# Kernel tuning notes

Hardware: AMD Instinct MI355X
Metric: run time of the kernel (lower is better)

Reference implementation:

```python
import jax, jax.numpy as jnp
import numpy as np

B, S, D_FEAT, K_PER_ID = 128, 32, 256, 8   # PK sampling: 16 ids x 8 instances
MARGIN, K_AP, K_AN = 0.3, 3, 6
EPS = 1e-12


def setup_inputs() -> dict:
    key = jax.random.key(0)
    inputs = jax.random.normal(key, (B, S, D_FEAT), dtype=jnp.float32)
    # PK-structured labels: each identity appears exactly K_PER_ID times so every
    # anchor has the same number of positives/negatives (required by the reshape(b,-1)).
    targets = jnp.repeat(jnp.arange(B // K_PER_ID, dtype=jnp.int32), K_PER_ID)
    return {"inputs": inputs, "targets": targets}


def _phd_loss(inputs, targets):
    b, s, d = inputs.shape
    # F.normalize(p=2, dim=-1)
    x = inputs / jnp.maximum(jnp.linalg.norm(inputs, axis=-1, keepdims=True), EPS)
    X = x.reshape(b * s, d)
    # pairwise euclidean distances, (bs, bs)
    sq = jnp.sum(X * X, axis=1)
    dist = jnp.sqrt(jnp.clip(sq[:, None] + sq[None, :] - 2.0 * (X @ X.T), EPS, None))
    # as_strided block view: D[i*b+j] = dist[i*s:(i+1)*s, j*s:(j+1)*s]
    D = dist.reshape(b, s, b, s).transpose(0, 2, 1, 3).reshape(b * b, s, s)
    # positive / negative block indices (constants w.r.t. autodiff)
    tgt = np.asarray(targets)
    m = (tgt[:, None] == tgt[None, :]).reshape(-1)
    pos = np.nonzero(m)[0]    # b * K entries, grouped by anchor (row-major)
    neg = np.nonzero(~m)[0]   # b * (b - K) entries
    # set-to-set distances: min over frames of the other tracklet
    dij = jnp.min(D, axis=1)  # (b*b, s)
    dji = jnp.min(D, axis=2)  # (b*b, s)
    # hard positive: k_ap-th largest frame-min per positive block, max over ij/ji, max over positives
    ap_ij = jax.lax.top_k(dij[pos], K_AP)[0][:, -1]
    ap_ji = jax.lax.top_k(dji[pos], K_AP)[0][:, -1]
    dist_ap = jnp.max(jnp.maximum(ap_ij, ap_ji).reshape(b, -1), axis=1)
    # hard negative: k_an-th largest frame-min per negative block, min over ij/ji, min over negatives
    an_ij = jax.lax.top_k(dij[neg], K_AN)[0][:, -1]
    an_ji = jax.lax.top_k(dji[neg], K_AN)[0][:, -1]
    dist_an = jnp.min(jnp.minimum(an_ij, an_ji).reshape(b, -1), axis=1)
    # MarginRankingLoss(margin)(dist_an, dist_ap, y=1), reduction='mean'
    return jnp.mean(jax.nn.relu(dist_ap - dist_an + MARGIN))


def reference(inputs, targets):
    return _phd_loss(inputs, targets)
```

## Files before the change

### kernel.cpp

```cpp
#include <hip/hip_runtime.h>
#include <hip/hip_bf16.h>

#define NB 128
#define NS 32
#define DF 256
#define NROW (NB*NS)
#define KSTEPS (DF/16)
#define MARGIN 0.3f
#define PANEL (KSTEPS*64)
#define NPAIR (NB*(NB+1)/2)

typedef short bf16x8 __attribute__((ext_vector_type(8)));
typedef short bf16x4 __attribute__((ext_vector_type(4)));
typedef float f32x16 __attribute__((ext_vector_type(16)));

__device__ __forceinline__ short f2bf(float x) {
    unsigned u = __float_as_uint(x);
    u += 0x7fffu + ((u >> 16) & 1u);
    return (short)(u >> 16);
}

__global__ __launch_bounds__(64) void norm_kernel(const float* __restrict__ in,
                                                  short* __restrict__ Xhi) {
    const int row = blockIdx.x;
    const int lane = threadIdx.x;
    const float4 v = ((const float4*)(in + (size_t)row * DF))[lane];
    float s = v.x*v.x + v.y*v.y + v.z*v.z + v.w*v.w;
    #pragma unroll
    for (int off = 32; off; off >>= 1) s += __shfl_xor(s, off);
    const float inv = 1.0f / fmaxf(sqrtf(s), 1e-12f);
    const float o[4] = {v.x*inv, v.y*inv, v.z*inv, v.w*inv};

    const int trk = row >> 5, r32 = row & 31;
    const int k4 = lane * 4;
    const int ks = k4 >> 4;
    const int kq = k4 & 15;
    const int tl = ((kq >> 3) << 5) | r32;
    const size_t off8 = ((size_t)(trk * KSTEPS + ks) * 64 + tl) * 8 + (kq & 7);

    bf16x4 hv;
    #pragma unroll
    for (int c = 0; c < 4; c++) hv[c] = f2bf(o[c]);
    *(bf16x4*)(Xhi + off8) = hv;
}

__global__ __launch_bounds__(256) void pair_kernel(const short* __restrict__ Xhi,
                                                   const int* __restrict__ tgt,
                                                   float* __restrict__ val) {
    const int w = threadIdx.x >> 6;
    const int l = threadIdx.x & 63;
    const int h = l >> 5;
    const int idx = blockIdx.x * 4 + w;

    int i = (int)(128.5f - sqrtf(128.5f * 128.5f - 2.0f * (float)idx));
    while ((i + 1) * NB - ((i + 1) * i) / 2 <= idx) ++i;
    while (i * NB - (i * (i - 1)) / 2 > idx) --i;
    const int j = i + (idx - (i * NB - (i * (i - 1)) / 2));

    const bf16x8* P = (const bf16x8*)Xhi;
    const bf16x8* A = P + (size_t)i * PANEL + l;
    const bf16x8* B = P + (size_t)j * PANEL + l;

    f32x16 accF, accR;
    #pragma unroll
    for (int r = 0; r < 16; r++) { accF[r] = 0.0f; accR[r] = 0.0f; }

    #pragma unroll
    for (int ks = 0; ks < KSTEPS; ks++) {
        const bf16x8 a = A[ks * 64];
        const bf16x8 b = B[ks * 64];
        accF = __builtin_amdgcn_mfma_f32_32x32x16_bf16(a, b, accF, 0, 0, 0);
        accR = __builtin_amdgcn_mfma_f32_32x32x16_bf16(b, a, accR, 0, 0, 0);
    }

    const bool pos = (tgt[i] == tgt[j]);
    const int K = pos ? 3 : 6;

    float cf = accF[0], cr = accR[0];
    #pragma unroll
    for (int r = 1; r < 16; r++) { cf = fmaxf(cf, accF[r]); cr = fmaxf(cr, accR[r]); }
    cf = fmaxf(cf, __shfl_xor(cf, 32));
    cr = fmaxf(cr, __shfl_xor(cr, 32));

    __shared__ float buf[4][64];
    __shared__ float kv[4][2];
    buf[w][l] = h ? cr : cf;

    const float x = buf[w][l];
    const float* cb = &buf[w][h * 32];
    int c = 0, e = 0;
    #pragma unroll
    for (int q = 0; q < 8; q++) {
        const float4 y = *(const float4*)(cb + 4 * q);
        c += (y.x < x) + (y.y < x) + (y.z < x) + (y.w < x);
        e += (y.x == x) + (y.y == x) + (y.z == x) + (y.w == x);
    }
    if (c < K && c + e >= K) kv[w][h] = x;

    if (l == 0) {
        const float aij = kv[w][0], aji = kv[w][1];
        const float ac = pos ? fminf(aij, aji) : fmaxf(aij, aji);
        const float d = sqrtf(fmaxf(2.0f - 2.0f * ac, 1e-12f));
        val[i * NB + j] = d;
        val[j * NB + i] = d;
    }
}

__global__ __launch_bounds__(1024) void reduce_kernel(const float* __restrict__ val,
                                                      const int* __restrict__ tgt,
                                                      float* __restrict__ out) {
    __shared__ int   tg[NB];
    __shared__ float ls[NB];
    const int tid = threadIdx.x;
    if (tid < NB) tg[tid] = tgt[tid];
    __syncthreads();

    const int i = tid >> 3;
    const int g = tid & 7;
    const int ti = tg[i];
    float ap = -1e30f, an = 1e30f;
    const float4* vp = (const float4*)(val + i * NB + g * 16);
    #pragma unroll
    for (int q = 0; q < 4; q++) {
        const float4 v = vp[q];
        const int jb = g * 16 + q * 4;
        if (tg[jb + 0] == ti) ap = fmaxf(ap, v.x); else an = fminf(an, v.x);
        if (tg[jb + 1] == ti) ap = fmaxf(ap, v.y); else an = fminf(an, v.y);
        if (tg[jb + 2] == ti) ap = fmaxf(ap, v.z); else an = fminf(an, v.z);
        if (tg[jb + 3] == ti) ap = fmaxf(ap, v.w); else an = fminf(an, v.w);
    }
    #pragma unroll
    for (int off = 1; off < 8; off <<= 1) {
        ap = fmaxf(ap, __shfl_xor(ap, off));
        an = fminf(an, __shfl_xor(an, off));
    }
    if (g == 0) ls[i] = fmaxf(ap - an + MARGIN, 0.0f);
    __syncthreads();

    if (tid < 64) {
        float li = ls[tid] + ls[tid + 64];
        #pragma unroll
        for (int off = 32; off; off >>= 1) li += __shfl_xor(li, off);
        if (tid == 0) out[0] = li * (1.0f / (float)NB);
    }
}

extern "C" void kernel_launch(void* const* d_in, const int* in_sizes, int n_in,
                              void* d_out, int out_size, void* d_ws, size_t ws_size,
                              hipStream_t stream) {
    const float* in = (const float*)d_in[0];
    const int* tgt = (const int*)d_in[1];
    float* out = (float*)d_out;

    short* Xhi = (short*)d_ws;
    float* val = (float*)(Xhi + (size_t)NROW * DF);

    norm_kernel<<<NROW, 64, 0, stream>>>(in, Xhi);
    pair_kernel<<<NPAIR / 4, 256, 0, stream>>>(Xhi, tgt, val);
    reduce_kernel<<<1, 1024, 0, stream>>>(val, tgt, out);
}
```

Before: 26.18 us.

## Fuse reduction into pair kernel via last-block ticket and tile pairs in 2x2 superblocks

Removes the separate reduce kernel: each pair block increments an atomic counter and the last block to finish performs the final loss reduction. Pair work is regrouped so each block handles a 2x2 superblock of tracklet pairs, giving some L2/cache reuse of panels, and the norm kernel now packs four rows per block. A memset of the counter is added per launch. The superblock scheme computes some redundant diagonal pairs (i>j within diagonal superblocks), but these write symmetric values and so stay correct.

```diff
diff --git a/kernel.cpp b/kernel.cpp
--- a/kernel.cpp
+++ b/kernel.cpp
@@ -8,7 +8,8 @@
 #define KSTEPS (DF/16)
 #define MARGIN 0.3f
 #define PANEL (KSTEPS*64)
-#define NPAIR (NB*(NB+1)/2)
+#define NSUP (NB/2)
+#define NSBLK (NSUP*(NSUP+1)/2)
 
 typedef short bf16x8 __attribute__((ext_vector_type(8)));
 typedef short bf16x4 __attribute__((ext_vector_type(4)));
@@ -20,10 +21,10 @@
     return (short)(u >> 16);
 }
 
-__global__ __launch_bounds__(64) void norm_kernel(const float* __restrict__ in,
-                                                  short* __restrict__ Xhi) {
-    const int row = blockIdx.x;
-    const int lane = threadIdx.x;
+__global__ __launch_bounds__(256) void norm_kernel(const float* __restrict__ in,
+                                                   short* __restrict__ Xhi) {
+    const int row = blockIdx.x * 4 + (threadIdx.x >> 6);
+    const int lane = threadIdx.x & 63;
     const float4 v = ((const float4*)(in + (size_t)row * DF))[lane];
     float s = v.x*v.x + v.y*v.y + v.z*v.z + v.w*v.w;
     #pragma unroll
@@ -46,16 +47,20 @@
 
 __global__ __launch_bounds__(256) void pair_kernel(const short* __restrict__ Xhi,
                                                    const int* __restrict__ tgt,
-                                                   float* __restrict__ val) {
+                                                   float* __restrict__ val,
+                                                   unsigned* __restrict__ cnt,
+                                                   float* __restrict__ out) {
     const int w = threadIdx.x >> 6;
     const int l = threadIdx.x & 63;
     const int h = l >> 5;
-    const int idx = blockIdx.x * 4 + w;
+    const int sidx = blockIdx.x;
 
-    int i = (int)(128.5f - sqrtf(128.5f * 128.5f - 2.0f * (float)idx));
-    while ((i + 1) * NB - ((i + 1) * i) / 2 <= idx) ++i;
-    while (i * NB - (i * (i - 1)) / 2 > idx) --i;
-    const int j = i + (idx - (i * NB - (i * (i - 1)) / 2));
+    int si = (int)(64.5f - sqrtf(64.5f * 64.5f - 2.0f * (float)sidx));
+    while ((si + 1) * NSUP - ((si + 1) * si) / 2 <= sidx) ++si;
+    while (si * NSUP - (si * (si - 1)) / 2 > sidx) --si;
+    const int sj = si + (sidx - (si * NSUP - (si * (si - 1)) / 2));
+    const int i = 2 * si + (w >> 1);
+    const int j = 2 * sj + (w & 1);
 
     const bf16x8* P = (const bf16x8*)Xhi;
     const bf16x8* A = P + (size_t)i * PANEL + l;
@@ -104,37 +109,41 @@
         val[i * NB + j] = d;
         val[j * NB + i] = d;
     }
-}
 
-__global__ __launch_bounds__(1024) void reduce_kernel(const float* __restrict__ val,
-                                                      const int* __restrict__ tgt,
-                                                      float* __restrict__ out) {
+    __shared__ unsigned ticket;
+    __syncthreads();
+    if (threadIdx.x == 0) {
+        __threadfence();
+        ticket = __hip_atomic_fetch_add(cnt, 1u, __ATOMIC_ACQ_REL,
+                                        __HIP_MEMORY_SCOPE_AGENT);
+    }
+    __syncthreads();
+    if (ticket != NSBLK - 1) return;
+    __threadfence();
+
     __shared__ int   tg[NB];
     __shared__ float ls[NB];
     const int tid = threadIdx.x;
     if (tid < NB) tg[tid] = tgt[tid];
     __syncthreads();
 
-    const int i = tid >> 3;
-    const int g = tid & 7;
-    const int ti = tg[i];
+    const int a  = tid >> 1;
+    const int hf = tid & 1;
+    const int ta = tg[a];
     float ap = -1e30f, an = 1e30f;
-    const float4* vp = (const float4*)(val + i * NB + g * 16);
+    const float4* vp = (const float4*)(val + a * NB + hf * 64);
     #pragma unroll
-    for (int q = 0; q < 4; q++) {
+    for (int q = 0; q < 16; q++) {
         const float4 v = vp[q];
-        const int jb = g * 16 + q * 4;
-        if (tg[jb + 0] == ti) ap = fmaxf(ap, v.x); else an = fminf(an, v.x);
-        if (tg[jb + 1] == ti) ap = fmaxf(ap, v.y); else an = fminf(an, v.y);
-        if (tg[jb + 2] == ti) ap = fmaxf(ap, v.z); else an = fminf(an, v.z);
-        if (tg[jb + 3] == ti) ap = fmaxf(ap, v.w); else an = fminf(an, v.w);
+        const int jb = hf * 64 + q * 4;
+        if (tg[jb + 0] == ta) ap = fmaxf(ap, v.x); else an = fminf(an, v.x);
+        if (tg[jb + 1] == ta) ap = fmaxf(ap, v.y); else an = fminf(an, v.y);
+        if (tg[jb + 2] == ta) ap = fmaxf(ap, v.z); else an = fminf(an, v.z);
+        if (tg[jb + 3] == ta) ap = fmaxf(ap, v.w); else an = fminf(an, v.w);
     }
-    #pragma unroll
-    for (int off = 1; off < 8; off <<= 1) {
-        ap = fmaxf(ap, __shfl_xor(ap, off));
-        an = fminf(an, __shfl_xor(an, off));
-    }
-    if (g == 0) ls[i] = fmaxf(ap - an + MARGIN, 0.0f);
+    ap = fmaxf(ap, __shfl_xor(ap, 1));
+    an = fminf(an, __shfl_xor(an, 1));
+    if (hf == 0) ls[a] = fmaxf(ap - an + MARGIN, 0.0f);
     __syncthreads();
 
     if (tid < 64) {
@@ -154,8 +163,9 @@
 
     short* Xhi = (short*)d_ws;
     float* val = (float*)(Xhi + (size_t)NROW * DF);
+    unsigned* cnt = (unsigned*)(val + NB * NB);
 
-    norm_kernel<<<NROW, 64, 0, stream>>>(in, Xhi);
-    pair_kernel<<<NPAIR / 4, 256, 0, stream>>>(Xhi, tgt, val);
-    reduce_kernel<<<1, 1024, 0, stream>>>(val, tgt, out);
+    hipMemsetAsync(cnt, 0, sizeof(unsigned), stream);
+    norm_kernel<<<NROW / 4, 256, 0, stream>>>(in, Xhi);
+    pair_kernel<<<NSBLK, 256, 0, stream>>>(Xhi, tgt, val, cnt, out);
 }
```

Result: slower. 100.6 us (+284.3%).
